# Kernel optimization log

Measured on AMD Instinct MI355X. Metric: run time of the kernel, lower is better.

## Reference

```python
import jax, jax.numpy as jnp
import numpy as np

N_NODES = 50000
N_EDGES = 600000
IN_DIM = 128
HID = 64
HEADS = 4
NEG_SLOPE = 0.2


def _glorot(key, shape):
    fan_in, fan_out = shape[0], shape[-1]
    lim = jnp.sqrt(6.0 / (fan_in + fan_out))
    return jax.random.uniform(key, shape, jnp.float32, -lim, lim)


def setup_inputs() -> dict:
    key = jax.random.key(0)
    ks = jax.random.split(key, 16)
    x = jax.random.normal(ks[0], (N_NODES, IN_DIM), jnp.float32)
    edge_index = jax.random.randint(ks[1], (2, N_EDGES), 0, N_NODES, jnp.int32)
    # GAT layer 1: in=128 -> heads=4, out=64, concat -> 256
    W1 = _glorot(ks[2], (IN_DIM, HEADS * HID))
    a_src1 = _glorot(ks[3], (HEADS, HID))
    a_dst1 = _glorot(ks[4], (HEADS, HID))
    b1 = jnp.zeros((HEADS * HID,), jnp.float32)
    # GAT layer 2: in=256 -> heads=1, out=64, no concat
    W2 = _glorot(ks[5], (HEADS * HID, 1 * HID))
    a_src2 = _glorot(ks[6], (1, HID))
    a_dst2 = _glorot(ks[7], (1, HID))
    b2 = jnp.zeros((HID,), jnp.float32)
    # classifier: Linear(64,32) -> ReLU -> Dropout(eval: identity) -> Linear(32,2)
    Wc1 = _glorot(ks[8], (HID, 32))
    bc1 = jnp.zeros((32,), jnp.float32)
    Wc2 = _glorot(ks[9], (32, 2))
    bc2 = jnp.zeros((2,), jnp.float32)
    return {"x": x, "edge_index": edge_index,
            "W1": W1, "a_src1": a_src1, "a_dst1": a_dst1, "b1": b1,
            "W2": W2, "a_src2": a_src2, "a_dst2": a_dst2, "b2": b2,
            "Wc1": Wc1, "bc1": bc1, "Wc2": Wc2, "bc2": bc2}


def _gat_conv(x, src, dst, W, a_src, a_dst, b, heads, out_ch, concat):
    N = x.shape[0]
    h = (x @ W).reshape(N, heads, out_ch)          # [N,H,C]
    alpha_s = jnp.sum(h * a_src, axis=-1)          # [N,H]
    alpha_d = jnp.sum(h * a_dst, axis=-1)          # [N,H]
    e = jax.nn.leaky_relu(alpha_s[src] + alpha_d[dst], NEG_SLOPE)  # [E,H]
    # segment softmax over edges grouped by destination node
    m = jax.ops.segment_max(e, dst, num_segments=N)                # [N,H]
    ex = jnp.exp(e - m[dst])
    denom = jax.ops.segment_sum(ex, dst, num_segments=N)           # [N,H]
    alpha = ex / (denom[dst] + 1e-16)                              # [E,H]
    msg = h[src] * alpha[:, :, None]                               # [E,H,C]
    out = jax.ops.segment_sum(msg, dst, num_segments=N)            # [N,H,C]
    out = out.reshape(N, heads * out_ch) if concat else out.mean(axis=1)
    return out + b


def reference(x, edge_index, W1, a_src1, a_dst1, b1, W2, a_src2, a_dst2, b2,
              Wc1, bc1, Wc2, bc2):
    N = x.shape[0]
    # PyG GATConv default add_self_loops=True (same augmented edge set both layers)
    loops = jnp.arange(N, dtype=edge_index.dtype)
    src = jnp.concatenate([edge_index[0], loops])
    dst = jnp.concatenate([edge_index[1], loops])
    h = _gat_conv(x, src, dst, W1, a_src1, a_dst1, b1, HEADS, HID, True)
    h = jax.nn.relu(h)
    h = _gat_conv(h, src, dst, W2, a_src2, a_dst2, b2, 1, HID, False)
    h = jax.nn.relu(h)
    h = jax.nn.relu(h @ Wc1 + bc1)   # Dropout(0.2) is identity in eval mode
    return h @ Wc2 + bc2
```

## Files before the change

kernel.cpp:

```cpp
#include <hip/hip_runtime.h>
#include <hip/hip_fp16.h>

#define N_NODES 50000
#define N_EDGESx 600000
#define E_TOT   (N_EDGESx + N_NODES)
#define NEG_SLOPE 0.2f

typedef _Float16 f16x4 __attribute__((ext_vector_type(4)));
typedef float f32x4 __attribute__((ext_vector_type(4)));

__device__ __forceinline__ float lrelu(float x) { return x > 0.f ? x : NEG_SLOPE * x; }

__global__ __launch_bounds__(256) void prepcnt_k(const float* __restrict__ W1,
                                                 const float* __restrict__ W2,
                                                 _Float16* __restrict__ Bt1,
                                                 _Float16* __restrict__ Bt2,
                                                 const int* __restrict__ ei,
                                                 int* __restrict__ counts) {
    int b = blockIdx.x;
    if (b < 32) {
        constexpr int K = 128, N = 256;
        int q = b * 256 + threadIdx.x;
        int n = q & (N - 1);
        int k4 = q / N;
        f16x4 v;
#pragma unroll
        for (int i = 0; i < 4; ++i)
            v[i] = (_Float16)W1[(size_t)(k4 * 4 + i) * N + n];
        int idx = n * K + (((k4 >> 1) ^ (n & 15)) << 3) + ((k4 & 1) << 2);
        *(f16x4*)&Bt1[idx] = v;
    } else if (b < 48) {
        constexpr int K = 256, N = 64;
        int q = (b - 32) * 256 + threadIdx.x;
        int n = q & (N - 1);
        int k4 = q / N;
        f16x4 v;
#pragma unroll
        for (int i = 0; i < 4; ++i) {
            int kg = k4 * 4 + i;
            int krow = (kg & 3) * 64 + (kg >> 2);
            v[i] = (_Float16)W2[(size_t)krow * N + n];
        }
        int idx = n * K + (((k4 >> 1) ^ (n & 15)) << 3) + ((k4 & 1) << 2);
        *(f16x4*)&Bt2[idx] = v;
    } else {
        int i = (b - 48) * 256 + threadIdx.x;
        if (i >= E_TOT) return;
        int dst = (i < N_EDGESx) ? ei[N_EDGESx + i] : (i - N_EDGESx);
        atomicAdd(&counts[dst], 1);
    }
}

__global__ __launch_bounds__(1024) void scanA(const int* __restrict__ counts,
                                              int* __restrict__ offs,
                                              int* __restrict__ chunks, int N) {
    __shared__ int sdata[1024];
    int t = threadIdx.x;
    int g = blockIdx.x * 1024 + t;
    int v = (g < N) ? counts[g] : 0;
    sdata[t] = v;
    __syncthreads();
    for (int off = 1; off < 1024; off <<= 1) {
        int x = (t >= off) ? sdata[t - off] : 0;
        __syncthreads();
        sdata[t] += x;
        __syncthreads();
    }
    int incl = sdata[t];
    if (g < N) offs[g] = incl - v;
    if (t == 1023) chunks[blockIdx.x] = incl;
}

__global__ void scanB(int* chunks, int nch) {
    int lane = threadIdx.x & 63;
    int orig = (lane < nch) ? chunks[lane] : 0;
    int v = orig;
#pragma unroll
    for (int off = 1; off < 64; off <<= 1) {
        int u = __shfl_up(v, off);
        if (lane >= off) v += u;
    }
    if (lane < nch) chunks[lane] = v - orig;
}

__global__ __launch_bounds__(1024) void scanC(int* __restrict__ offs,
                                              const int* __restrict__ chunks, int N) {
    int g = blockIdx.x * 1024 + threadIdx.x;
    if (g < N) offs[g] += chunks[blockIdx.x];
}

__global__ __launch_bounds__(256) void scatter_k(const int* __restrict__ ei,
                                                 const int* __restrict__ offs,
                                                 int* __restrict__ cursor,
                                                 int* __restrict__ edge_src) {
    int i = blockIdx.x * 256 + threadIdx.x;
    if (i >= E_TOT) return;
    int src, dst;
    if (i < N_EDGESx) { src = ei[i]; dst = ei[N_EDGESx + i]; }
    else              { src = dst = i - N_EDGESx; }
    int pos = atomicAdd(&cursor[dst], 1);
    edge_src[offs[dst] + pos] = src;
}

template<int K, int N, int CPW, typename AT, int CPERM, int ALPHA>
__global__ __launch_bounds__(256, 2) void gemm_mfma(const AT* __restrict__ A,
                                                    const _Float16* __restrict__ Bt,
                                                    _Float16* __restrict__ C,
                                                    const float* __restrict__ asrc,
                                                    const float* __restrict__ adst,
                                                    float* __restrict__ as_o,
                                                    float* __restrict__ ad_o, int M) {
    __shared__ __align__(16) _Float16 Ah[64 * K];
    __shared__ __align__(16) _Float16 Bh[N * K];
    const int t = threadIdx.x;
    const int row0 = blockIdx.x * 64;

#pragma unroll
    for (int q = t; q < 64 * K / 4; q += 256) {
        int r = q / (K / 4);
        int k4 = q % (K / 4);
        f16x4 v;
        int grow = row0 + r;
        if (grow < M) {
            if constexpr (sizeof(AT) == 4) {
                float4 f = *(const float4*)(A + (size_t)grow * K + k4 * 4);
                v[0] = (_Float16)f.x; v[1] = (_Float16)f.y;
                v[2] = (_Float16)f.z; v[3] = (_Float16)f.w;
            } else {
                v = *(const f16x4*)(A + (size_t)grow * K + k4 * 4);
            }
        } else {
            v[0] = v[1] = v[2] = v[3] = (_Float16)0.f;
        }
        int idx = r * K + (((k4 >> 1) ^ (r & 15)) << 3) + ((k4 & 1) << 2);
        *(f16x4*)&Ah[idx] = v;
    }
#pragma unroll
    for (int q = t; q < N * K / 8; q += 256)
        ((uint4*)Bh)[q] = ((const uint4*)Bt)[q];
    __syncthreads();

    const int w = t >> 6;
    const int l = t & 63;
    const int lr = l & 15;
    const int g = l >> 4;

    f32x4 acc[4][CPW];
#pragma unroll
    for (int mt = 0; mt < 4; ++mt)
#pragma unroll
        for (int nt = 0; nt < CPW; ++nt)
            acc[mt][nt] = (f32x4){0.f, 0.f, 0.f, 0.f};

#pragma unroll
    for (int ks = 0; ks < K / 16; ++ks) {
        int k = ks * 16 + g * 4;
        f16x4 a[4], b[CPW];
#pragma unroll
        for (int mt = 0; mt < 4; ++mt) {
            int r = mt * 16 + lr;
            a[mt] = *(const f16x4*)&Ah[r * K + (((k >> 3) ^ (r & 15)) << 3) + (k & 7)];
        }
#pragma unroll
        for (int nt = 0; nt < CPW; ++nt) {
            int n = (w * CPW + nt) * 16 + lr;
            b[nt] = *(const f16x4*)&Bh[n * K + (((k >> 3) ^ (n & 15)) << 3) + (k & 7)];
        }
#pragma unroll
        for (int mt = 0; mt < 4; ++mt)
#pragma unroll
            for (int nt = 0; nt < CPW; ++nt)
                acc[mt][nt] = __builtin_amdgcn_mfma_f32_16x16x16f16(a[mt], b[nt],
                                                                   acc[mt][nt], 0, 0, 0);
    }

    if constexpr (CPERM) {
        float* A_s  = (float*)Ah;
        float* A_d  = A_s + 256;
        float* psum = A_d + 256;
        __syncthreads();
        _Float16* Cs = Bh;
#pragma unroll
        for (int mt = 0; mt < 4; ++mt)
#pragma unroll
            for (int q = 0; q < 4; ++q) {
                int row = mt * 16 + g * 4 + q;
#pragma unroll
                for (int nt = 0; nt < CPW; ++nt) {
                    int gcol = (w * CPW + nt) * 16 + lr;
                    int ocol = ((gcol & 63) << 2) | (gcol >> 6);
                    Cs[row * N + ocol] = (_Float16)acc[mt][nt][q];
                }
            }
        if constexpr (ALPHA == 1) { A_s[t] = asrc[t]; A_d[t] = adst[t]; }
        __syncthreads();
#pragma unroll
        for (int q = t; q < 64 * N / 8; q += 256) {
            int row = q / (N / 8);
            int c8 = q % (N / 8);
            int grow = row0 + row;
            if (grow < M)
                *(float4*)(C + (size_t)grow * N + c8 * 8) =
                    *(const float4*)&Cs[row * N + c8 * 8];
        }
        if constexpr (ALPHA == 1) {
            int row = t & 63, qr = t >> 6;
            float s[4] = {}, d[4] = {};
#pragma unroll
            for (int j = 0; j < 16; ++j) {
                int c = qr * 16 + j;
                union { uint2 u; __half h[4]; } U;
                U.u = *(const uint2*)&Cs[row * 256 + c * 4];
#pragma unroll
                for (int h = 0; h < 4; ++h) {
                    float f = __half2float(U.h[h]);
                    s[h] += f * A_s[h * 64 + c];
                    d[h] += f * A_d[h * 64 + c];
                }
            }
            float* ps = psum + (row * 4 + qr) * 8;
#pragma unroll
            for (int h = 0; h < 4; ++h) { ps[h] = s[h]; ps[4 + h] = d[h]; }
            __syncthreads();
            if (t < 64 && row0 + t < M) {
                float4 S = make_float4(0.f, 0.f, 0.f, 0.f);
                float4 D = make_float4(0.f, 0.f, 0.f, 0.f);
#pragma unroll
                for (int q2 = 0; q2 < 4; ++q2) {
                    float* ps2 = psum + (t * 4 + q2) * 8;
                    S.x += ps2[0]; S.y += ps2[1]; S.z += ps2[2]; S.w += ps2[3];
                    D.x += ps2[4]; D.y += ps2[5]; D.z += ps2[6]; D.w += ps2[7];
                }
                *(float4*)(as_o + (size_t)(row0 + t) * 4) = S;
                *(float4*)(ad_o + (size_t)(row0 + t) * 4) = D;
            }
        }
    } else {
#pragma unroll
        for (int mt = 0; mt < 4; ++mt)
#pragma unroll
            for (int q = 0; q < 4; ++q) {
                int grow = row0 + mt * 16 + g * 4 + q;
                if (grow >= M) continue;
#pragma unroll
                for (int nt = 0; nt < CPW; ++nt) {
                    int gcol = (w * CPW + nt) * 16 + lr;
                    C[(size_t)grow * N + gcol] = (_Float16)acc[mt][nt][q];
                }
            }
        if constexpr (ALPHA == 2) {
            __half* Ch  = (__half*)Ah;
            float*  A_s = (float*)(Ch + 64 * 64);
            float*  A_d = A_s + 64;
            float*  psum = A_d + 64;
            __syncthreads();
#pragma unroll
            for (int mt = 0; mt < 4; ++mt)
#pragma unroll
                for (int q = 0; q < 4; ++q) {
                    int row = mt * 16 + g * 4 + q;
                    Ch[row * 64 + w * 16 + lr] = __float2half(acc[mt][0][q]);
                }
            if (t < 64) { A_s[t] = asrc[t]; A_d[t] = adst[t]; }
            __syncthreads();
            int row = t & 63, qr = t >> 6;
            float s = 0.f, d = 0.f;
#pragma unroll
            for (int j = 0; j < 16; ++j) {
                int c = qr * 16 + j;
                float f = __half2float(Ch[row * 64 + c]);
                s += f * A_s[c];
                d += f * A_d[c];
            }
            psum[(row * 4 + qr) * 2]     = s;
            psum[(row * 4 + qr) * 2 + 1] = d;
            __syncthreads();
            if (t < 64 && row0 + t < M) {
                float S = 0.f, D = 0.f;
#pragma unroll
                for (int q2 = 0; q2 < 4; ++q2) {
                    S += psum[(t * 4 + q2) * 2];
                    D += psum[(t * 4 + q2) * 2 + 1];
                }
                as_o[row0 + t] = S;
                ad_o[row0 + t] = D;
            }
        }
    }
}

__global__ __launch_bounds__(256) void stats1w_k(const int* __restrict__ edge_src,
                                                 const float* __restrict__ as1,
                                                 const float* __restrict__ ad1,
                                                 const int* __restrict__ offs,
                                                 const int* __restrict__ counts,
                                                 __half* __restrict__ w4, int N) {
    int t = threadIdx.x;
    int l16 = t & 15;
    int n = blockIdx.x * 16 + (t >> 4);
    if (n >= N) return;
    int start = offs[n];
    int end = start + counts[n];
    int h4 = l16 & 3;
    float4 ad = *(const float4*)(ad1 + (size_t)n * 4);
    float adh = h4 == 0 ? ad.x : h4 == 1 ? ad.y : h4 == 2 ? ad.z : ad.w;
    float m = -1e30f, s = 0.f;
    for (int p = start + (l16 >> 2); p < end; p += 4) {
        float e = lrelu(as1[(size_t)edge_src[p] * 4 + h4] + adh);
        float nm = fmaxf(m, e);
        s = s * __expf(m - nm) + __expf(e - nm);
        m = nm;
    }
#pragma unroll
    for (int i = 0; i < 2; ++i) {
        int msk = 4 << i;
        float om = __shfl_xor(m, msk);
        float os = __shfl_xor(s, msk);
        float nm = fmaxf(m, om);
        s = s * __expf(m - nm) + os * __expf(om - nm);
        m = nm;
    }
    float rcp = 1.f / (s + 1e-16f);
    int gb = (t & 63) & ~15;
    float4 mh = make_float4(__shfl(m, gb), __shfl(m, gb + 1), __shfl(m, gb + 2), __shfl(m, gb + 3));
    float4 rs = make_float4(__shfl(rcp, gb), __shfl(rcp, gb + 1), __shfl(rcp, gb + 2), __shfl(rcp, gb + 3));
    for (int p = start + l16; p < end; p += 16) {
        float4 a = *(const float4*)(as1 + (size_t)edge_src[p] * 4);
        union { uint2 u; __half h[4]; } W;
        W.h[0] = __float2half(__expf(lrelu(a.x + ad.x) - mh.x) * rs.x);
        W.h[1] = __float2half(__expf(lrelu(a.y + ad.y) - mh.y) * rs.y);
        W.h[2] = __float2half(__expf(lrelu(a.z + ad.z) - mh.z) * rs.z);
        W.h[3] = __float2half(__expf(lrelu(a.w + ad.w) - mh.w) * rs.w);
        *(uint2*)(w4 + (size_t)p * 4) = W.u;
    }
}

__global__ __launch_bounds__(256) void stats2w_k(const int* __restrict__ edge_src,
                                                 const float* __restrict__ as2,
                                                 const float* __restrict__ ad2,
                                                 const int* __restrict__ offs,
                                                 const int* __restrict__ counts,
                                                 __half* __restrict__ w2, int N) {
    int t = threadIdx.x;
    int l16 = t & 15;
    int n = blockIdx.x * 16 + (t >> 4);
    if (n >= N) return;
    int start = offs[n];
    int end = start + counts[n];
    float adn = ad2[n];
    float m = -1e30f, s = 0.f;
    for (int p = start + l16; p < end; p += 16) {
        float e = lrelu(as2[edge_src[p]] + adn);
        float nm = fmaxf(m, e);
        s = s * __expf(m - nm) + __expf(e - nm);
        m = nm;
    }
#pragma unroll
    for (int i = 0; i < 4; ++i) {
        int msk = 1 << i;
        float om = __shfl_xor(m, msk);
        float os = __shfl_xor(s, msk);
        float nm = fmaxf(m, om);
        s = s * __expf(m - nm) + os * __expf(om - nm);
        m = nm;
    }
    float rn = 1.f / (s + 1e-16f);
    for (int p = start + l16; p < end; p += 16)
        w2[p] = __float2half(__expf(lrelu(as2[edge_src[p]] + adn) - m) * rn);
}

__global__ __launch_bounds__(256) void agg1_k(const __half* __restrict__ h1,
                                              const __half* __restrict__ w4,
                                              const int* __restrict__ edge_src,
                                              const int* __restrict__ offs,
                                              const int* __restrict__ counts,
                                              const float* __restrict__ b1,
                                              __half* __restrict__ out1, int N) {
    int lane = threadIdx.x & 63;
    int n = blockIdx.x * 4 + (threadIdx.x >> 6);
    if (n >= N) return;
    int start = offs[n];
    int end = start + counts[n];
    float acc0 = 0.f, acc1 = 0.f, acc2 = 0.f, acc3 = 0.f;
    int p = start;
    for (; p + 7 < end; p += 8) {
        int s[8]; uint2 hw[8], ww[8];
#pragma unroll
        for (int i = 0; i < 8; ++i) s[i] = edge_src[p + i];
#pragma unroll
        for (int i = 0; i < 8; ++i) ww[i] = *(const uint2*)(w4 + (size_t)(p + i) * 4);
#pragma unroll
        for (int i = 0; i < 8; ++i) hw[i] = *(const uint2*)(h1 + (size_t)s[i] * 256 + lane * 4);
#pragma unroll
        for (int i = 0; i < 8; ++i) {
            union { uint2 u; __half h[4]; } U, W;
            U.u = hw[i]; W.u = ww[i];
            acc0 += __half2float(U.h[0]) * __half2float(W.h[0]);
            acc1 += __half2float(U.h[1]) * __half2float(W.h[1]);
            acc2 += __half2float(U.h[2]) * __half2float(W.h[2]);
            acc3 += __half2float(U.h[3]) * __half2float(W.h[3]);
        }
    }
    for (; p < end; ++p) {
        int s0 = edge_src[p];
        union { uint2 u; __half h[4]; } U0, W0;
        W0.u = *(const uint2*)(w4 + (size_t)p * 4);
        U0.u = *(const uint2*)(h1 + (size_t)s0 * 256 + lane * 4);
        acc0 += __half2float(U0.h[0]) * __half2float(W0.h[0]);
        acc1 += __half2float(U0.h[1]) * __half2float(W0.h[1]);
        acc2 += __half2float(U0.h[2]) * __half2float(W0.h[2]);
        acc3 += __half2float(U0.h[3]) * __half2float(W0.h[3]);
    }
    union { uint2 u; __half h[4]; } O;
    O.h[0] = __float2half(fmaxf(acc0 + b1[lane], 0.f));
    O.h[1] = __float2half(fmaxf(acc1 + b1[64 + lane], 0.f));
    O.h[2] = __float2half(fmaxf(acc2 + b1[128 + lane], 0.f));
    O.h[3] = __float2half(fmaxf(acc3 + b1[192 + lane], 0.f));
    *(uint2*)(out1 + (size_t)n * 256 + lane * 4) = O.u;
}

__global__ __launch_bounds__(256) void agg2_k(const __half* __restrict__ h2,
                                              const __half* __restrict__ w2,
                                              const int* __restrict__ edge_src,
                                              const int* __restrict__ offs,
                                              const int* __restrict__ counts,
                                              const float* __restrict__ b2,
                                              __half* __restrict__ out2, int N) {
    int t = threadIdx.x;
    int l16 = t & 15;
    int n = blockIdx.x * 16 + (t >> 4);
    if (n >= N) return;
    int start = offs[n];
    int end = start + counts[n];
    float a0 = 0.f, a1 = 0.f, a2 = 0.f, a3 = 0.f;
    int p = start;
    for (; p + 7 < end; p += 8) {
        int s[8]; __half wv8[8]; uint2 hv8[8];
#pragma unroll
        for (int i = 0; i < 8; ++i) s[i] = edge_src[p + i];
#pragma unroll
        for (int i = 0; i < 8; ++i) wv8[i] = w2[p + i];
#pragma unroll
        for (int i = 0; i < 8; ++i)
            hv8[i] = *(const uint2*)(h2 + (size_t)s[i] * 64 + l16 * 4);
#pragma unroll
        for (int i = 0; i < 8; ++i) {
            union { uint2 u; __half h[4]; } U;
            U.u = hv8[i];
            float w = __half2float(wv8[i]);
            a0 += __half2float(U.h[0]) * w;
            a1 += __half2float(U.h[1]) * w;
            a2 += __half2float(U.h[2]) * w;
            a3 += __half2float(U.h[3]) * w;
        }
    }
    for (; p < end; ++p) {
        int s0 = edge_src[p];
        union { uint2 u; __half h[4]; } U;
        U.u = *(const uint2*)(h2 + (size_t)s0 * 64 + l16 * 4);
        float w = __half2float(w2[p]);
        a0 += __half2float(U.h[0]) * w;
        a1 += __half2float(U.h[1]) * w;
        a2 += __half2float(U.h[2]) * w;
        a3 += __half2float(U.h[3]) * w;
    }
    union { uint2 u; __half h[4]; } O;
    O.h[0] = __float2half(fmaxf(a0 + b2[l16 * 4],     0.f));
    O.h[1] = __float2half(fmaxf(a1 + b2[l16 * 4 + 1], 0.f));
    O.h[2] = __float2half(fmaxf(a2 + b2[l16 * 4 + 2], 0.f));
    O.h[3] = __float2half(fmaxf(a3 + b2[l16 * 4 + 3], 0.f));
    *(uint2*)(out2 + (size_t)n * 64 + l16 * 4) = O.u;
}

__global__ __launch_bounds__(256) void cls_k(const __half* __restrict__ hin,
                                             const float* __restrict__ Wc1,
                                             const float* __restrict__ bc1,
                                             const float* __restrict__ Wc2,
                                             const float* __restrict__ bc2,
                                             float* __restrict__ out, int N) {
    __shared__ float W1s[64 * 32];
    __shared__ float W2s[64];
    __shared__ float b1s[32];
    __shared__ float b2s[2];
    __shared__ float z[8][33];
    int t = threadIdx.x;
    for (int i = t; i < 2048; i += 256) W1s[i] = Wc1[i];
    if (t < 64) W2s[t] = Wc2[t];
    if (t < 32) b1s[t] = bc1[t];
    if (t < 2)  b2s[t] = bc2[t];
    __syncthreads();
    int nl = t >> 5, j = t & 31;
    int n = blockIdx.x * 8 + nl;
    float acc = b1s[j];
    if (n < N) {
        const __half* hr = hin + (size_t)n * 64;
#pragma unroll 8
        for (int l = 0; l < 64; ++l) acc += __half2float(hr[l]) * W1s[l * 32 + j];
    }
    z[nl][j] = fmaxf(acc, 0.f);
    __syncthreads();
    if (j < 2 && n < N) {
        float o = b2s[j];
#pragma unroll
        for (int q = 0; q < 32; ++q) o += z[nl][q] * W2s[q * 2 + j];
        out[(size_t)n * 2 + j] = o;
    }
}

extern "C" void kernel_launch(void* const* d_in, const int* in_sizes, int n_in,
                              void* d_out, int out_size, void* d_ws, size_t ws_size,
                              hipStream_t stream) {
    const float* x      = (const float*)d_in[0];
    const int*   ei     = (const int*)d_in[1];
    const float* W1     = (const float*)d_in[2];
    const float* a_src1 = (const float*)d_in[3];
    const float* a_dst1 = (const float*)d_in[4];
    const float* b1     = (const float*)d_in[5];
    const float* W2     = (const float*)d_in[6];
    const float* a_src2 = (const float*)d_in[7];
    const float* a_dst2 = (const float*)d_in[8];
    const float* b2     = (const float*)d_in[9];
    const float* Wc1    = (const float*)d_in[10];
    const float* bc1    = (const float*)d_in[11];
    const float* Wc2    = (const float*)d_in[12];
    const float* bc2    = (const float*)d_in[13];

    char* ws = (char*)d_ws;
    size_t off = 0;
    auto alloc = [&](size_t bytes) -> void* {
        void* p = ws + off;
        off += (bytes + 255) & ~(size_t)255;
        return p;
    };
    int*       counts   = (int*)alloc((size_t)N_NODES * 4);
    int*       cursor   = (int*)alloc((size_t)N_NODES * 4);
    int*       offs     = (int*)alloc((size_t)N_NODES * 4);
    int*       chunks   = (int*)alloc(256);
    int*       edge_src = (int*)alloc((size_t)E_TOT * 4);
    float*     as1      = (float*)alloc((size_t)N_NODES * 16);
    float*     ad1      = (float*)alloc((size_t)N_NODES * 16);
    float*     as2      = (float*)alloc((size_t)N_NODES * 4);
    float*     ad2      = (float*)alloc((size_t)N_NODES * 4);
    __half*    w4       = (__half*)alloc((size_t)E_TOT * 8);
    _Float16*  Bt1      = (_Float16*)alloc((size_t)256 * 128 * 2);
    _Float16*  Bt2      = (_Float16*)alloc((size_t)64 * 256 * 2);
    __half*    h1h      = (__half*)alloc((size_t)N_NODES * 256 * 2);
    __half*    out1h    = (__half*)alloc((size_t)N_NODES * 256 * 2);
    __half*    out2h    = (__half*)alloc((size_t)N_NODES * 64 * 2);
    __half*    h2h  = h1h;
    __half*    w2b  = w4;

    const int EB = (E_TOT + 255) / 256;
    const int NB4 = (N_NODES + 3) / 4;
    const int NB16 = (N_NODES + 15) / 16;
    const int NCH = (N_NODES + 1023) / 1024;
    const int MB = (N_NODES + 63) / 64;

    hipMemsetAsync(counts, 0, (char*)cursor - (char*)counts + (size_t)N_NODES * 4, stream);

    prepcnt_k<<<48 + EB, 256, 0, stream>>>(W1, W2, Bt1, Bt2, ei, counts);
    scanA<<<NCH, 1024, 0, stream>>>(counts, offs, chunks, N_NODES);
    scanB<<<1, 64, 0, stream>>>(chunks, NCH);
    scanC<<<NCH, 1024, 0, stream>>>(offs, chunks, N_NODES);
    scatter_k<<<EB, 256, 0, stream>>>(ei, offs, cursor, edge_src);

    gemm_mfma<128, 256, 4, float, 1, 1><<<MB, 256, 0, stream>>>(
        x, Bt1, (_Float16*)h1h, a_src1, a_dst1, as1, ad1, N_NODES);
    stats1w_k<<<NB16, 256, 0, stream>>>(edge_src, as1, ad1, offs, counts, w4, N_NODES);
    agg1_k<<<NB4, 256, 0, stream>>>(h1h, w4, edge_src, offs, counts, b1, out1h, N_NODES);

    gemm_mfma<256, 64, 1, _Float16, 0, 2><<<MB, 256, 0, stream>>>(
        (const _Float16*)out1h, Bt2, (_Float16*)h2h, a_src2, a_dst2, as2, ad2, N_NODES);
    stats2w_k<<<NB16, 256, 0, stream>>>(edge_src, as2, ad2, offs, counts, w2b, N_NODES);
    agg2_k<<<NB16, 256, 0, stream>>>(h2h, w2b, edge_src, offs, counts, b2, out2h, N_NODES);

    cls_k<<<N_NODES / 8, 256, 0, stream>>>(out2h, Wc1, bc1, Wc2, bc2, (float*)d_out, N_NODES);
}
```

Before: 235.0 us.

## Fuse chunk scan into scanC and cache gathered attention scores in stats kernels

Removes the single-wave scanB launch by having each scanC block recompute the chunk prefix itself in its first wavefront. In stats1w_k, each lane now gathers full float4 source scores per edge and tracks four per-head online softmax states, so the score read is vectorized and not split by head. Both stats kernels keep the first four gathered scores in registers so the normalize pass can skip re-reading edge_src and the score array for low-degree nodes. This adds register pressure and predicated loop iterations.

```diff
diff --git a/kernel.cpp b/kernel.cpp
--- a/kernel.cpp
+++ b/kernel.cpp
@@ -71,22 +71,25 @@
     if (t == 1023) chunks[blockIdx.x] = incl;
 }
 
-__global__ void scanB(int* chunks, int nch) {
-    int lane = threadIdx.x & 63;
-    int orig = (lane < nch) ? chunks[lane] : 0;
-    int v = orig;
-#pragma unroll
-    for (int off = 1; off < 64; off <<= 1) {
-        int u = __shfl_up(v, off);
-        if (lane >= off) v += u;
-    }
-    if (lane < nch) chunks[lane] = v - orig;
-}
-
 __global__ __launch_bounds__(1024) void scanC(int* __restrict__ offs,
-                                              const int* __restrict__ chunks, int N) {
-    int g = blockIdx.x * 1024 + threadIdx.x;
-    if (g < N) offs[g] += chunks[blockIdx.x];
+                                              const int* __restrict__ chunks,
+                                              int N, int nch) {
+    __shared__ int base_s;
+    int t = threadIdx.x;
+    if (t < 64) {
+        int lane = t;
+        int orig = (lane < nch) ? chunks[lane] : 0;
+        int v = orig;
+#pragma unroll
+        for (int off = 1; off < 64; off <<= 1) {
+            int u = __shfl_up(v, off);
+            if (lane >= off) v += u;
+        }
+        if (lane == (int)blockIdx.x) base_s = v - orig;
+    }
+    __syncthreads();
+    int g = blockIdx.x * 1024 + t;
+    if (g < N) offs[g] += base_s;
 }
 
 __global__ __launch_bounds__(256) void scatter_k(const int* __restrict__ ei,
@@ -301,37 +304,57 @@
     if (n >= N) return;
     int start = offs[n];
     int end = start + counts[n];
-    int h4 = l16 & 3;
     float4 ad = *(const float4*)(ad1 + (size_t)n * 4);
-    float adh = h4 == 0 ? ad.x : h4 == 1 ? ad.y : h4 == 2 ? ad.z : ad.w;
-    float m = -1e30f, s = 0.f;
-    for (int p = start + (l16 >> 2); p < end; p += 4) {
-        float e = lrelu(as1[(size_t)edge_src[p] * 4 + h4] + adh);
-        float nm = fmaxf(m, e);
-        s = s * __expf(m - nm) + __expf(e - nm);
-        m = nm;
-    }
-#pragma unroll
-    for (int i = 0; i < 2; ++i) {
-        int msk = 4 << i;
-        float om = __shfl_xor(m, msk);
-        float os = __shfl_xor(s, msk);
-        float nm = fmaxf(m, om);
-        s = s * __expf(m - nm) + os * __expf(om - nm);
-        m = nm;
-    }
-    float rcp = 1.f / (s + 1e-16f);
-    int gb = (t & 63) & ~15;
-    float4 mh = make_float4(__shfl(m, gb), __shfl(m, gb + 1), __shfl(m, gb + 2), __shfl(m, gb + 3));
-    float4 rs = make_float4(__shfl(rcp, gb), __shfl(rcp, gb + 1), __shfl(rcp, gb + 2), __shfl(rcp, gb + 3));
-    for (int p = start + l16; p < end; p += 16) {
-        float4 a = *(const float4*)(as1 + (size_t)edge_src[p] * 4);
-        union { uint2 u; __half h[4]; } W;
-        W.h[0] = __float2half(__expf(lrelu(a.x + ad.x) - mh.x) * rs.x);
-        W.h[1] = __float2half(__expf(lrelu(a.y + ad.y) - mh.y) * rs.y);
-        W.h[2] = __float2half(__expf(lrelu(a.z + ad.z) - mh.z) * rs.z);
-        W.h[3] = __float2half(__expf(lrelu(a.w + ad.w) - mh.w) * rs.w);
-        *(uint2*)(w4 + (size_t)p * 4) = W.u;
+    float4 aa[4];
+    float m0 = -1e30f, m1 = -1e30f, m2 = -1e30f, m3 = -1e30f;
+    float s0 = 0.f, s1 = 0.f, s2 = 0.f, s3 = 0.f;
+    int nr = 0;
+    for (int p0 = start; p0 < end; p0 += 16, ++nr) {
+        int p = p0 + l16;
+        float4 a = make_float4(0.f, 0.f, 0.f, 0.f);
+        float e0 = -1e30f, e1 = -1e30f, e2 = -1e30f, e3 = -1e30f;
+        float val = 0.f;
+        if (p < end) {
+            a = *(const float4*)(as1 + (size_t)edge_src[p] * 4);
+            e0 = lrelu(a.x + ad.x); e1 = lrelu(a.y + ad.y);
+            e2 = lrelu(a.z + ad.z); e3 = lrelu(a.w + ad.w);
+            val = 1.f;
+        }
+        if (nr < 4) aa[nr] = a;
+        float nm;
+        nm = fmaxf(m0, e0); s0 = s0 * __expf(m0 - nm) + val * __expf(e0 - nm); m0 = nm;
+        nm = fmaxf(m1, e1); s1 = s1 * __expf(m1 - nm) + val * __expf(e1 - nm); m1 = nm;
+        nm = fmaxf(m2, e2); s2 = s2 * __expf(m2 - nm) + val * __expf(e2 - nm); m2 = nm;
+        nm = fmaxf(m3, e3); s3 = s3 * __expf(m3 - nm) + val * __expf(e3 - nm); m3 = nm;
+    }
+#pragma unroll
+    for (int i = 0; i < 4; ++i) {
+        int msk = 1 << i;
+        float om, os, nm;
+        om = __shfl_xor(m0, msk); os = __shfl_xor(s0, msk);
+        nm = fmaxf(m0, om); s0 = s0 * __expf(m0 - nm) + os * __expf(om - nm); m0 = nm;
+        om = __shfl_xor(m1, msk); os = __shfl_xor(s1, msk);
+        nm = fmaxf(m1, om); s1 = s1 * __expf(m1 - nm) + os * __expf(om - nm); m1 = nm;
+        om = __shfl_xor(m2, msk); os = __shfl_xor(s2, msk);
+        nm = fmaxf(m2, om); s2 = s2 * __expf(m2 - nm) + os * __expf(om - nm); m2 = nm;
+        om = __shfl_xor(m3, msk); os = __shfl_xor(s3, msk);
+        nm = fmaxf(m3, om); s3 = s3 * __expf(m3 - nm) + os * __expf(om - nm); m3 = nm;
+    }
+    float r0 = 1.f / (s0 + 1e-16f), r1 = 1.f / (s1 + 1e-16f);
+    float r2 = 1.f / (s2 + 1e-16f), r3 = 1.f / (s3 + 1e-16f);
+    nr = 0;
+    for (int p0 = start; p0 < end; p0 += 16, ++nr) {
+        int p = p0 + l16;
+        if (p < end) {
+            float4 a = (nr < 4) ? aa[nr]
+                                : *(const float4*)(as1 + (size_t)edge_src[p] * 4);
+            union { uint2 u; __half h[4]; } W;
+            W.h[0] = __float2half(__expf(lrelu(a.x + ad.x) - m0) * r0);
+            W.h[1] = __float2half(__expf(lrelu(a.y + ad.y) - m1) * r1);
+            W.h[2] = __float2half(__expf(lrelu(a.z + ad.z) - m2) * r2);
+            W.h[3] = __float2half(__expf(lrelu(a.w + ad.w) - m3) * r3);
+            *(uint2*)(w4 + (size_t)p * 4) = W.u;
+        }
     }
 }
 
@@ -348,11 +371,20 @@
     int start = offs[n];
     int end = start + counts[n];
     float adn = ad2[n];
+    float av[4];
     float m = -1e30f, s = 0.f;
-    for (int p = start + l16; p < end; p += 16) {
-        float e = lrelu(as2[edge_src[p]] + adn);
+    int nr = 0;
+    for (int p0 = start; p0 < end; p0 += 16, ++nr) {
+        int p = p0 + l16;
+        float a = 0.f, e = -1e30f, val = 0.f;
+        if (p < end) {
+            a = as2[edge_src[p]];
+            e = lrelu(a + adn);
+            val = 1.f;
+        }
+        if (nr < 4) av[nr] = a;
         float nm = fmaxf(m, e);
-        s = s * __expf(m - nm) + __expf(e - nm);
+        s = s * __expf(m - nm) + val * __expf(e - nm);
         m = nm;
     }
 #pragma unroll
@@ -365,8 +397,14 @@
         m = nm;
     }
     float rn = 1.f / (s + 1e-16f);
-    for (int p = start + l16; p < end; p += 16)
-        w2[p] = __float2half(__expf(lrelu(as2[edge_src[p]] + adn) - m) * rn);
+    nr = 0;
+    for (int p0 = start; p0 < end; p0 += 16, ++nr) {
+        int p = p0 + l16;
+        if (p < end) {
+            float a = (nr < 4) ? av[nr] : as2[edge_src[p]];
+            w2[p] = __float2half(__expf(lrelu(a + adn) - m) * rn);
+        }
+    }
 }
 
 __global__ __launch_bounds__(256) void agg1_k(const __half* __restrict__ h1,
@@ -560,8 +598,7 @@
 
     prepcnt_k<<<48 + EB, 256, 0, stream>>>(W1, W2, Bt1, Bt2, ei, counts);
     scanA<<<NCH, 1024, 0, stream>>>(counts, offs, chunks, N_NODES);
-    scanB<<<1, 64, 0, stream>>>(chunks, NCH);
-    scanC<<<NCH, 1024, 0, stream>>>(offs, chunks, N_NODES);
+    scanC<<<NCH, 1024, 0, stream>>>(offs, chunks, N_NODES, NCH);
     scatter_k<<<EB, 256, 0, stream>>>(ei, offs, cursor, edge_src);
 
     gemm_mfma<128, 256, 4, float, 1, 1><<<MB, 256, 0, stream>>>(
```

Result: no change. 235.6 us (+0.3%).
